# Kernel tuning notes

Measured on AMD Instinct MI355X. Metric: run time of the kernel, lower is better.

Reference implementation:

```python
import jax, jax.numpy as jnp
import numpy as np

N, LT, LV, D, H = 4, 1024, 1024, 1024, 16
HD = D // H
EPS = 1e-12


def layernorm(x, w, b):
    u = x.mean(-1, keepdims=True)
    s = ((x - u) ** 2).mean(-1, keepdims=True)
    return w * (x - u) / jnp.sqrt(s + EPS) + b


def attention(q_in, k_in, v_in, mask, qw, qb, kw, kb, vw, vb):
    # mask: (N, Lq_or_1, Lk) float in {0,1}; torch Linear is x @ W.T + b
    def heads(x, w, b):
        y = x @ w.T + b
        return y.reshape(y.shape[0], y.shape[1], H, HD).transpose(0, 2, 1, 3)  # (N,H,L,hd)
    q, k, v = heads(q_in, qw, qb), heads(k_in, kw, kb), heads(v_in, vw, vb)
    scores = jnp.einsum('bhqd,bhkd->bhqk', q, k) / np.sqrt(HD).astype(np.float32)
    scores = scores + (1.0 - mask[:, None]) * (-10000.0)
    probs = jax.nn.softmax(scores, axis=-1)  # dropout is identity in eval
    ctx = jnp.einsum('bhqk,bhkd->bhqd', probs, v)
    return ctx.transpose(0, 2, 1, 3).reshape(q_in.shape[0], q_in.shape[1], D)


def setup_inputs() -> dict:
    key = jax.random.key(0)
    ks = jax.random.split(key, 16)
    inp = {
        'dec_hidden_states': jax.random.normal(ks[0], (N, LT, D), jnp.float32),
        'enc_outputs': jax.random.normal(ks[1], (N, LV, D), jnp.float32),
        'dec_mask': jnp.ones((N, LT), jnp.float32),
        'enc_mask': jnp.ones((N, LV), jnp.float32),
    }
    wnames = ['sa_qw', 'sa_kw', 'sa_vw', 'ca_qw', 'ca_kw', 'ca_vw', 'out_w']
    for i, n in enumerate(wnames):
        inp[n] = jax.random.normal(ks[2 + i], (D, D), jnp.float32) * 0.02
    for n in ['sa_qb', 'sa_kb', 'sa_vb', 'ca_qb', 'ca_kb', 'ca_vb', 'out_b', 'n1_b', 'n2_b', 'out_ln_b']:
        inp[n] = jnp.zeros((D,), jnp.float32)
    for n in ['n1_w', 'n2_w', 'out_ln_w']:
        inp[n] = jnp.ones((D,), jnp.float32)
    return inp


def reference(dec_hidden_states, enc_outputs, dec_mask, enc_mask,
              sa_qw, sa_qb, sa_kw, sa_kb, sa_vw, sa_vb, n1_w, n1_b,
              ca_qw, ca_qb, ca_kw, ca_kb, ca_vw, ca_vb, n2_w, n2_b,
              out_w, out_b, out_ln_w, out_ln_b):
    Lt = dec_mask.shape[1]
    # diagonal_mask=True: causal tril combined with padding mask
    self_mask = dec_mask[:, None, :] * jnp.tril(jnp.ones((Lt, Lt), dec_mask.dtype))  # (N,Lt,Lt)
    a = attention(dec_hidden_states, dec_hidden_states, dec_hidden_states, self_mask,
                  sa_qw, sa_qb, sa_kw, sa_kb, sa_vw, sa_vb)
    a = layernorm(a + dec_hidden_states, n1_w, n1_b)
    c = attention(a, enc_outputs, enc_outputs, enc_mask[:, None, :],
                  ca_qw, ca_qb, ca_kw, ca_kb, ca_vw, ca_vb)
    c = layernorm(a + c, n2_w, n2_b)
    # BertOutput called as output(x, x): dense, residual, LN (dropout = identity)
    h = c @ out_w.T + out_b
    return layernorm(h + c, out_ln_w, out_ln_b)
```

## Files before the change

### kernel.cpp

```cpp
#include <hip/hip_runtime.h>
#include <cstdint>
#include <cstddef>

typedef __bf16 bf16x8 __attribute__((ext_vector_type(8)));
typedef float  floatx4 __attribute__((ext_vector_type(4)));
typedef unsigned short ushortx8 __attribute__((ext_vector_type(8)));
typedef unsigned short ushortx4 __attribute__((ext_vector_type(4)));

#define MFMA16(a, b, c) __builtin_amdgcn_mfma_f32_16x16x32_bf16((a), (b), (c), 0, 0, 0)

__device__ inline unsigned short f2bf(float f) {
    unsigned int u = __float_as_uint(f);
    unsigned int r = (u + 0x7fffu + ((u >> 16) & 1u)) >> 16;
    return (unsigned short)r;
}
__device__ inline float bf2f(unsigned short u) {
    return __uint_as_float(((unsigned int)u) << 16);
}

struct Src2 { const float* p[2]; };
__global__ __launch_bounds__(256) void k_x2_to_bf16(Src2 s2, unsigned short* __restrict__ dst) {
    int i = blockIdx.x * 256 + threadIdx.x;
    const float* src = s2.p[i >> 19];
    int off = i & 524287;
    const float4* s = (const float4*)src + (size_t)off * 2;
    float4 x0 = s[0], x1 = s[1];
    ushortx8 o;
    o[0] = f2bf(x0.x); o[1] = f2bf(x0.y); o[2] = f2bf(x0.z); o[3] = f2bf(x0.w);
    o[4] = f2bf(x1.x); o[5] = f2bf(x1.y); o[6] = f2bf(x1.z); o[7] = f2bf(x1.w);
    *((ushortx8*)dst + i) = o;
}
struct Src7 { const float* p[7]; };
__global__ __launch_bounds__(256) void k_w7_to_bf16(Src7 s7, unsigned short* __restrict__ dst) {
    int i = blockIdx.x * 256 + threadIdx.x;
    const float* src = s7.p[i >> 17];
    int off = i & 131071;
    const float4* s = (const float4*)src + (size_t)off * 2;
    float4 x0 = s[0], x1 = s[1];
    ushortx8 o;
    o[0] = f2bf(x0.x); o[1] = f2bf(x0.y); o[2] = f2bf(x0.z); o[3] = f2bf(x0.w);
    o[4] = f2bf(x1.x); o[5] = f2bf(x1.y); o[6] = f2bf(x1.z); o[7] = f2bf(x1.w);
    *((ushortx8*)dst + i) = o;
}

template <int MODE>
__global__ __launch_bounds__(256) void k_gemm_bias(const unsigned short* __restrict__ A,
                                                   const unsigned short* __restrict__ A2,
                                                   const unsigned short* __restrict__ W,
                                                   const float* __restrict__ bias0,
                                                   const float* __restrict__ bias1,
                                                   const float* __restrict__ bias2,
                                                   void* __restrict__ d0,
                                                   void* __restrict__ d1,
                                                   void* __restrict__ d2,
                                                   int K) {
    __shared__ __align__(16) unsigned short As[128 * 32];
    __shared__ __align__(16) unsigned short Bs[128 * 32];
    const int tid = threadIdx.x;
    const int wave = tid >> 6, lane = tid & 63;
    const int quad = lane >> 4, l15 = lane & 15;
    const int wm = wave >> 1, wn = wave & 1;
    const int m0 = blockIdx.x * 128, n0 = blockIdx.y * 128;
    const int sect_blk = n0 >> 10;

    const unsigned short* Ause = (MODE == 4 && sect_blk != 0) ? A2 : A;

    const size_t rowbytes = (size_t)K * 2;
    const int idx0 = tid, idx1 = 256 + tid;
    const int rA0 = idx0 >> 2, cb0 = (idx0 & 3) << 4;
    const int rA1 = idx1 >> 2, cb1 = (idx1 & 3) << 4;
    const char* gA0 = (const char*)Ause + (size_t)(m0 + rA0) * rowbytes + cb0;
    const char* gA1 = (const char*)Ause + (size_t)(m0 + rA1) * rowbytes + cb1;
    const char* gB0 = (const char*)W + (size_t)(n0 + rA0) * rowbytes + cb0;
    const char* gB1 = (const char*)W + (size_t)(n0 + rA1) * rowbytes + cb1;

    int4 pa0 = *(const int4*)gA0, pa1 = *(const int4*)gA1;
    int4 pb0 = *(const int4*)gB0, pb1 = *(const int4*)gB1;

    floatx4 acc[4][4] = {};

    const int KT = K >> 5;
    for (int kt = 0; kt < KT; ++kt) {
        __syncthreads();
        ((int4*)As)[idx0] = pa0; ((int4*)As)[idx1] = pa1;
        ((int4*)Bs)[idx0] = pb0; ((int4*)Bs)[idx1] = pb1;
        __syncthreads();
        if (kt + 1 < KT) {
            gA0 += 64; gA1 += 64; gB0 += 64; gB1 += 64;
            pa0 = *(const int4*)gA0; pa1 = *(const int4*)gA1;
            pb0 = *(const int4*)gB0; pb1 = *(const int4*)gB1;
        }
        bf16x8 af[4], bfr[4];
        const char* Asb = (const char*)As;
        const char* Bsb = (const char*)Bs;
#pragma unroll
        for (int r = 0; r < 4; ++r)
            af[r] = *(const bf16x8*)(Asb + ((wm * 64 + r * 16 + l15) * 64 + quad * 16));
#pragma unroll
        for (int c = 0; c < 4; ++c)
            bfr[c] = *(const bf16x8*)(Bsb + ((wn * 64 + c * 16 + l15) * 64 + quad * 16));
#pragma unroll
        for (int r = 0; r < 4; ++r)
#pragma unroll
            for (int c = 0; c < 4; ++c)
                acc[r][c] = MFMA16(af[r], bfr[c], acc[r][c]);
    }

#pragma unroll
    for (int c = 0; c < 4; ++c) {
        int col = n0 + wn * 64 + c * 16 + l15;
        int sect = col >> 10, cc = col & 1023;
        float bv;
        if (MODE == 3) bv = bias0[col];
        else bv = (sect == 0 ? bias0 : (sect == 1 ? bias1 : bias2))[cc];
        int h = cc >> 6, d = cc & 63;
#pragma unroll
        for (int r = 0; r < 4; ++r) {
            int mrow = m0 + wm * 64 + r * 16 + quad * 4;
#pragma unroll
            for (int i = 0; i < 4; ++i) {
                float v = acc[r][c][i] + bv;
                int row = mrow + i;
                if (MODE == 3) {
                    ((float*)d0)[(size_t)row * 1024 + col] = v;
                } else {
                    int b = row >> 10, l = row & 1023;
                    unsigned short* base = (unsigned short*)(sect == 0 ? d0 : (sect == 1 ? d1 : d2));
                    bool isV = (sect == 2);
                    size_t off;
                    if (isV) off = (size_t)(b * 16 + h) * 65536 + (size_t)(l >> 5) * 2048 + d * 32 + (l & 31);
                    else off = ((size_t)(b * 16 + h) * 1024 + l) * 64 + d;
                    base[off] = f2bf(v);
                }
            }
        }
    }
}

__global__ __launch_bounds__(256) void k_flash_attn(const unsigned short* __restrict__ Qp,
                                                    const unsigned short* __restrict__ Kp,
                                                    const unsigned short* __restrict__ Vp,
                                                    const float* __restrict__ mask,
                                                    float* __restrict__ ctx,
                                                    int causal) {
    const int L = 1024, D = 1024;
    int f = blockIdx.x;
    int qi = ((f >> 3) + (f >> 7)) & 15;
    int bh = (f & 7) + ((f >> 7) << 3);
    int h = bh & 15, b = bh >> 4;
    int tid = threadIdx.x;
    int wave = tid >> 6, lane = tid & 63, quad = lane >> 4, l15 = lane & 15;
    int qbase = qi * 64 + wave * 16;

    __shared__ __align__(16) unsigned short Ks[4096];
    __shared__ __align__(16) unsigned short Vs[5120];
    __shared__ unsigned short penb[1024];
    __shared__ __align__(16) unsigned short Plds[4][1280];

    {
        float4 mv = ((const float4*)(mask + b * L))[tid];
        ushortx4 pv;
        pv[0] = f2bf((1.0f - mv.x) * -10000.0f);
        pv[1] = f2bf((1.0f - mv.y) * -10000.0f);
        pv[2] = f2bf((1.0f - mv.z) * -10000.0f);
        pv[3] = f2bf((1.0f - mv.w) * -10000.0f);
        *((ushortx4*)penb + tid) = pv;
    }

    const unsigned short* Qh = Qp + ((size_t)(b * 16 + h) * 1024 + qbase) * 64;
    bf16x8 qf0 = *(const bf16x8*)(Qh + l15 * 64 + quad * 8);
    bf16x8 qf1 = *(const bf16x8*)(Qh + l15 * 64 + 32 + quad * 8);

    const char* Kh = (const char*)(Kp + (size_t)(b * 16 + h) * 65536);
    const char* Vh = (const char*)(Vp + (size_t)(b * 16 + h) * 65536);

    int ktiles = causal ? (qi + 1) : 16;

    char* Ksb = (char*)Ks;
    char* Vsb = (char*)Vs;
    int krow = tid >> 3, kblk = tid & 7;
    int kd0 = krow * 128 + ((kblk ^ (krow & 7)) << 4);
    int kd1 = kd0 + 32 * 128;
    int vd0 = (tid >> 2) * 80 + ((tid & 3) << 4);
    int vd1 = vd0 + 5120;

    int karA[4], karB[4];
#pragma unroll
    for (int r = 0; r < 4; ++r) {
        int row = r * 16 + l15;
        karA[r] = row * 128 + ((quad ^ (l15 & 7)) << 4);
        karB[r] = row * 128 + (((quad | 4) ^ (l15 & 7)) << 4);
    }
    int var_[8];
#pragma unroll
    for (int s = 0; s < 2; ++s)
#pragma unroll
        for (int fi = 0; fi < 4; ++fi)
            var_[s * 4 + fi] = s * 5120 + (fi * 16 + l15) * 80 + (quad << 4);

    floatx4 O[4] = {};
    float lsum[4] = {0.f, 0.f, 0.f, 0.f};
    unsigned short* pw_lo = &Plds[wave][0];
    unsigned short* pw_hi = &Plds[wave][640];

    int4 ka0 = *(const int4*)(Kh + tid * 16);
    int4 ka1 = *(const int4*)(Kh + 4096 + tid * 16);
    int4 va0 = *(const int4*)(Vh + tid * 16);
    int4 va1 = *(const int4*)(Vh + 4096 + tid * 16);

    for (int kt = 0; kt < ktiles; ++kt) {
        *(int4*)(Ksb + kd0) = ka0;
        *(int4*)(Ksb + kd1) = ka1;
        *(int4*)(Vsb + vd0) = va0;
        *(int4*)(Vsb + vd1) = va1;
        __syncthreads();
        if (kt + 1 < ktiles) {
            const char* Kg = Kh + (size_t)(kt + 1) * 8192;
            const char* Vg = Vh + (size_t)(kt + 1) * 8192;
            ka0 = *(const int4*)(Kg + tid * 16);
            ka1 = *(const int4*)(Kg + 4096 + tid * 16);
            va0 = *(const int4*)(Vg + tid * 16);
            va1 = *(const int4*)(Vg + 4096 + tid * 16);
        }
        int k0 = kt * 64;

        floatx4 S0 = {}, S1 = {}, S2 = {}, S3 = {};
        {
            bf16x8 kA0 = *(const bf16x8*)(Ksb + karA[0]);
            bf16x8 kB0 = *(const bf16x8*)(Ksb + karB[0]);
            bf16x8 kA1 = *(const bf16x8*)(Ksb + karA[1]);
            bf16x8 kB1 = *(const bf16x8*)(Ksb + karB[1]);
            S0 = MFMA16(qf0, kA0, S0); S0 = MFMA16(qf1, kB0, S0);
            S1 = MFMA16(qf0, kA1, S1); S1 = MFMA16(qf1, kB1, S1);
            bf16x8 kA2 = *(const bf16x8*)(Ksb + karA[2]);
            bf16x8 kB2 = *(const bf16x8*)(Ksb + karB[2]);
            bf16x8 kA3 = *(const bf16x8*)(Ksb + karA[3]);
            bf16x8 kB3 = *(const bf16x8*)(Ksb + karB[3]);
            S2 = MFMA16(qf0, kA2, S2); S2 = MFMA16(qf1, kB2, S2);
            S3 = MFMA16(qf0, kA3, S3); S3 = MFMA16(qf1, kB3, S3);
        }

        float pen0 = bf2f(penb[k0 + l15]);
        float pen1 = bf2f(penb[k0 + 16 + l15]);
        float pen2 = bf2f(penb[k0 + 32 + l15]);
        float pen3 = bf2f(penb[k0 + 48 + l15]);

#pragma unroll
        for (int i = 0; i < 4; ++i) {
            float e0, e1, e2, e3;
            if (causal) {
                int q = qbase + quad * 4 + i;
                e0 = ((k0 + l15) <= q) ? pen0 : -10000.0f;
                e1 = ((k0 + 16 + l15) <= q) ? pen1 : -10000.0f;
                e2 = ((k0 + 32 + l15) <= q) ? pen2 : -10000.0f;
                e3 = ((k0 + 48 + l15) <= q) ? pen3 : -10000.0f;
            } else {
                e0 = pen0; e1 = pen1; e2 = pen2; e3 = pen3;
            }
            float p0 = __expf(fmaf(S0[i], 0.125f, e0));
            float p1 = __expf(fmaf(S1[i], 0.125f, e1));
            float p2 = __expf(fmaf(S2[i], 0.125f, e2));
            float p3 = __expf(fmaf(S3[i], 0.125f, e3));
            lsum[i] += (p0 + p1) + (p2 + p3);
            int ro = (quad * 4 + i) * 40;
            pw_lo[ro + l15] = f2bf(p0);
            pw_lo[ro + 16 + l15] = f2bf(p1);
            pw_hi[ro + l15] = f2bf(p2);
            pw_hi[ro + 16 + l15] = f2bf(p3);
        }

        bf16x8 pa_lo = *(const bf16x8*)(pw_lo + l15 * 40 + quad * 8);
        bf16x8 pa_hi = *(const bf16x8*)(pw_hi + l15 * 40 + quad * 8);
        bf16x8 v0 = *(const bf16x8*)(Vsb + var_[0]);
        bf16x8 v1 = *(const bf16x8*)(Vsb + var_[1]);
        bf16x8 v2 = *(const bf16x8*)(Vsb + var_[2]);
        bf16x8 v3 = *(const bf16x8*)(Vsb + var_[3]);
        O[0] = MFMA16(pa_lo, v0, O[0]);
        O[1] = MFMA16(pa_lo, v1, O[1]);
        O[2] = MFMA16(pa_lo, v2, O[2]);
        O[3] = MFMA16(pa_lo, v3, O[3]);
        bf16x8 v4 = *(const bf16x8*)(Vsb + var_[4]);
        bf16x8 v5 = *(const bf16x8*)(Vsb + var_[5]);
        bf16x8 v6 = *(const bf16x8*)(Vsb + var_[6]);
        bf16x8 v7 = *(const bf16x8*)(Vsb + var_[7]);
        O[0] = MFMA16(pa_hi, v4, O[0]);
        O[1] = MFMA16(pa_hi, v5, O[1]);
        O[2] = MFMA16(pa_hi, v6, O[2]);
        O[3] = MFMA16(pa_hi, v7, O[3]);
        __syncthreads();
    }

#pragma unroll
    for (int i = 0; i < 4; ++i) {
        float l = lsum[i];
        l += __shfl_xor(l, 1);
        l += __shfl_xor(l, 2);
        l += __shfl_xor(l, 4);
        l += __shfl_xor(l, 8);
        float inv = 1.0f / l;
        int q = qbase + quad * 4 + i;
        float* op = ctx + ((size_t)(b * L + q)) * D + h * 64;
#pragma unroll
        for (int fi = 0; fi < 4; ++fi) op[fi * 16 + l15] = O[fi][i] * inv;
    }
}

__global__ __launch_bounds__(256) void k_add_ln(const float* __restrict__ X,
                                                const float* __restrict__ Y,
                                                const float* __restrict__ w,
                                                const float* __restrict__ bvec,
                                                float* __restrict__ outf,
                                                unsigned short* __restrict__ outbf) {
    int row = blockIdx.x;
    int tid = threadIdx.x;
    float4 x = *((const float4*)(X + (size_t)row * 1024) + tid);
    float4 y = *((const float4*)(Y + (size_t)row * 1024) + tid);
    float v0 = x.x + y.x, v1 = x.y + y.y, v2 = x.z + y.z, v3 = x.w + y.w;
    float s = v0 + v1 + v2 + v3;
    float s2 = v0 * v0 + v1 * v1 + v2 * v2 + v3 * v3;
#pragma unroll
    for (int off = 32; off > 0; off >>= 1) {
        s += __shfl_xor(s, off);
        s2 += __shfl_xor(s2, off);
    }
    __shared__ float red[8];
    int wave = tid >> 6, lane = tid & 63;
    if (lane == 0) { red[wave] = s; red[4 + wave] = s2; }
    __syncthreads();
    s = red[0] + red[1] + red[2] + red[3];
    s2 = red[4] + red[5] + red[6] + red[7];
    float u = s * (1.0f / 1024.0f);
    float var = s2 * (1.0f / 1024.0f) - u * u;
    float r = 1.0f / sqrtf(fmaxf(var, 0.0f) + 1e-12f);
    float4 wv = *((const float4*)w + tid);
    float4 bv = *((const float4*)bvec + tid);
    float o0 = wv.x * (v0 - u) * r + bv.x;
    float o1 = wv.y * (v1 - u) * r + bv.y;
    float o2 = wv.z * (v2 - u) * r + bv.z;
    float o3 = wv.w * (v3 - u) * r + bv.w;
    float4 o = {o0, o1, o2, o3};
    *((float4*)(outf + (size_t)row * 1024) + tid) = o;
    if (outbf) {
        ushortx4 ob;
        ob[0] = f2bf(o0); ob[1] = f2bf(o1); ob[2] = f2bf(o2); ob[3] = f2bf(o3);
        *((ushortx4*)outbf + (size_t)row * 256 + tid) = ob;
    }
}

extern "C" void kernel_launch(void* const* d_in, const int* in_sizes, int n_in,
                              void* d_out, int out_size, void* d_ws, size_t ws_size,
                              hipStream_t stream) {
    (void)in_sizes; (void)n_in; (void)out_size; (void)ws_size;
    const float* dec = (const float*)d_in[0];
    const float* enc = (const float*)d_in[1];
    const float* dec_mask = (const float*)d_in[2];
    const float* enc_mask = (const float*)d_in[3];
    const float* b_saq = (const float*)d_in[11];
    const float* b_sak = (const float*)d_in[12];
    const float* b_sav = (const float*)d_in[13];
    const float* b_caq = (const float*)d_in[14];
    const float* b_cak = (const float*)d_in[15];
    const float* b_cav = (const float*)d_in[16];
    const float* b_out = (const float*)d_in[17];
    const float* n1_b = (const float*)d_in[18];
    const float* n2_b = (const float*)d_in[19];
    const float* oln_b = (const float*)d_in[20];
    const float* n1_w = (const float*)d_in[21];
    const float* n2_w = (const float*)d_in[22];
    const float* oln_w = (const float*)d_in[23];

    char* ws = (char*)d_ws;
    const size_t MB2 = 2097152;
    const size_t ACT_BF = 8388608;
    const size_t ACT_F32 = 16777216;
    unsigned short* Wbf[7];
    for (int i = 0; i < 7; ++i) Wbf[i] = (unsigned short*)(ws + i * MB2);
    size_t off = 7 * MB2;
    unsigned short* Xbf = (unsigned short*)(ws + off); off += ACT_BF;
    unsigned short* Ebf = (unsigned short*)(ws + off); off += ACT_BF;
    unsigned short* Abf = (unsigned short*)(ws + off); off += ACT_BF;
    unsigned short* Cbf = (unsigned short*)(ws + off); off += ACT_BF;
    unsigned short* Qp = (unsigned short*)(ws + off); off += ACT_BF;
    unsigned short* Kp = (unsigned short*)(ws + off); off += ACT_BF;
    unsigned short* Vp = (unsigned short*)(ws + off); off += ACT_BF;
    float* ctx = (float*)(ws + off); off += ACT_F32;
    float* a_f32 = (float*)(ws + off); off += ACT_F32;
    float* c_f32 = (float*)(ws + off); off += ACT_F32;
    float* h_f32 = ctx;
    float* outp = (float*)d_out;

    dim3 blk(256);
    dim3 attn_grid(1024);

    Src2 s2; s2.p[0] = dec; s2.p[1] = enc;
    k_x2_to_bf16<<<dim3(4096), blk, 0, stream>>>(s2, Xbf);
    Src7 s7;
    for (int i = 0; i < 7; ++i) s7.p[i] = (const float*)d_in[4 + i];
    k_w7_to_bf16<<<dim3(3584), blk, 0, stream>>>(s7, Wbf[0]);

    k_gemm_bias<0><<<dim3(32, 24), blk, 0, stream>>>(Xbf, Xbf, Wbf[0], b_saq, b_sak, b_sav,
                                                     Qp, Kp, Vp, 1024);
    k_flash_attn<<<attn_grid, blk, 0, stream>>>(Qp, Kp, Vp, dec_mask, ctx, 1);
    k_add_ln<<<dim3(4096), blk, 0, stream>>>(ctx, dec, n1_w, n1_b, a_f32, Abf);

    k_gemm_bias<4><<<dim3(32, 24), blk, 0, stream>>>(Abf, Ebf, Wbf[3], b_caq, b_cak, b_cav,
                                                     Qp, Kp, Vp, 1024);
    k_flash_attn<<<attn_grid, blk, 0, stream>>>(Qp, Kp, Vp, enc_mask, ctx, 0);
    k_add_ln<<<dim3(4096), blk, 0, stream>>>(a_f32, ctx, n2_w, n2_b, c_f32, Cbf);

    k_gemm_bias<3><<<dim3(32, 8), blk, 0, stream>>>(Cbf, Cbf, Wbf[6], b_out, b_out, b_out,
                                                    h_f32, nullptr, nullptr, 1024);
    k_add_ln<<<dim3(4096), blk, 0, stream>>>(h_f32, c_f32, oln_w, oln_b, outp, (unsigned short*)nullptr);
}
```

Baseline: 351.0 us.

## Double query rows per attention wave, reuse K/V fragments, use exp2 softmax

The flash-attention kernel now handles 128 query rows per block (32 per wave, split into two 16-row halves). Each K/V fragment loaded from LDS is reused for both halves, and the grid is halved. Softmax switches to exp2 with a log2e-prescaled score and float mask penalty. P is packed into bf16 pairs with a perm instruction, and V is stored with a permuted key order to match. Causal tiles and halves that are fully masked are skipped. The risk is higher register pressure, hence launch_bounds(256,2), and fewer blocks for the GPU to schedule.

```diff
diff --git a/kernel.cpp b/kernel.cpp
--- a/kernel.cpp
+++ b/kernel.cpp
@@ -13,9 +13,6 @@
     unsigned int u = __float_as_uint(f);
     unsigned int r = (u + 0x7fffu + ((u >> 16) & 1u)) >> 16;
     return (unsigned short)r;
-}
-__device__ inline float bf2f(unsigned short u) {
-    return __uint_as_float(((unsigned int)u) << 16);
 }
 
 struct Src2 { const float* p[2]; };
@@ -128,8 +125,13 @@
                     unsigned short* base = (unsigned short*)(sect == 0 ? d0 : (sect == 1 ? d1 : d2));
                     bool isV = (sect == 2);
                     size_t off;
-                    if (isV) off = (size_t)(b * 16 + h) * 65536 + (size_t)(l >> 5) * 2048 + d * 32 + (l & 31);
-                    else off = ((size_t)(b * 16 + h) * 1024 + l) * 64 + d;
+                    if (isV) {
+                        int kk = l & 31;
+                        int kperm = ((kk & 15) << 1) | (kk >> 4);
+                        off = (size_t)(b * 16 + h) * 65536 + (size_t)(l >> 5) * 2048 + d * 32 + kperm;
+                    } else {
+                        off = ((size_t)(b * 16 + h) * 1024 + l) * 64 + d;
+                    }
                     base[off] = f2bf(v);
                 }
             }
@@ -137,44 +139,50 @@
     }
 }
 
-__global__ __launch_bounds__(256) void k_flash_attn(const unsigned short* __restrict__ Qp,
-                                                    const unsigned short* __restrict__ Kp,
-                                                    const unsigned short* __restrict__ Vp,
-                                                    const float* __restrict__ mask,
-                                                    float* __restrict__ ctx,
-                                                    int causal) {
+__global__ __launch_bounds__(256, 2) void k_flash_attn(const unsigned short* __restrict__ Qp,
+                                                       const unsigned short* __restrict__ Kp,
+                                                       const unsigned short* __restrict__ Vp,
+                                                       const float* __restrict__ mask,
+                                                       float* __restrict__ ctx,
+                                                       int causal) {
     const int L = 1024, D = 1024;
+    const float SC = 0.18033688011112042f;
     int f = blockIdx.x;
-    int qi = ((f >> 3) + (f >> 7)) & 15;
-    int bh = (f & 7) + ((f >> 7) << 3);
+    int g = f >> 6;
+    int bh = (f & 7) + (g << 3);
+    int qt = ((f >> 3) + g) & 7;
     int h = bh & 15, b = bh >> 4;
     int tid = threadIdx.x;
     int wave = tid >> 6, lane = tid & 63, quad = lane >> 4, l15 = lane & 15;
-    int qbase = qi * 64 + wave * 16;
+    int qbase = qt * 128 + wave * 32;
 
     __shared__ __align__(16) unsigned short Ks[4096];
     __shared__ __align__(16) unsigned short Vs[5120];
-    __shared__ unsigned short penb[1024];
-    __shared__ __align__(16) unsigned short Plds[4][1280];
+    __shared__ float penf[1024];
+    __shared__ __align__(16) unsigned short Plds[4 * 1280];
 
     {
         float4 mv = ((const float4*)(mask + b * L))[tid];
-        ushortx4 pv;
-        pv[0] = f2bf((1.0f - mv.x) * -10000.0f);
-        pv[1] = f2bf((1.0f - mv.y) * -10000.0f);
-        pv[2] = f2bf((1.0f - mv.z) * -10000.0f);
-        pv[3] = f2bf((1.0f - mv.w) * -10000.0f);
-        *((ushortx4*)penb + tid) = pv;
+        float4 pv;
+        pv.x = (1.0f - mv.x) * -14426.950408889634f;
+        pv.y = (1.0f - mv.y) * -14426.950408889634f;
+        pv.z = (1.0f - mv.z) * -14426.950408889634f;
+        pv.w = (1.0f - mv.w) * -14426.950408889634f;
+        ((float4*)penf)[tid] = pv;
     }
 
     const unsigned short* Qh = Qp + ((size_t)(b * 16 + h) * 1024 + qbase) * 64;
-    bf16x8 qf0 = *(const bf16x8*)(Qh + l15 * 64 + quad * 8);
-    bf16x8 qf1 = *(const bf16x8*)(Qh + l15 * 64 + 32 + quad * 8);
+    bf16x8 qf[2][2];
+#pragma unroll
+    for (int qh = 0; qh < 2; ++qh) {
+        qf[qh][0] = *(const bf16x8*)(Qh + (qh * 16 + l15) * 64 + quad * 8);
+        qf[qh][1] = *(const bf16x8*)(Qh + (qh * 16 + l15) * 64 + 32 + quad * 8);
+    }
 
     const char* Kh = (const char*)(Kp + (size_t)(b * 16 + h) * 65536);
     const char* Vh = (const char*)(Vp + (size_t)(b * 16 + h) * 65536);
 
-    int ktiles = causal ? (qi + 1) : 16;
+    int ktiles = causal ? (2 * qt + 2) : 16;
 
     char* Ksb = (char*)Ks;
     char* Vsb = (char*)Vs;
@@ -198,10 +206,10 @@
         for (int fi = 0; fi < 4; ++fi)
             var_[s * 4 + fi] = s * 5120 + (fi * 16 + l15) * 80 + (quad << 4);
 
-    floatx4 O[4] = {};
-    float lsum[4] = {0.f, 0.f, 0.f, 0.f};
-    unsigned short* pw_lo = &Plds[wave][0];
-    unsigned short* pw_hi = &Plds[wave][640];
+    floatx4 O[2][4] = {};
+    float lsum[2][4] = {};
+    unsigned short* pw = &Plds[wave * 1280];
+    unsigned int* pw32 = (unsigned int*)pw;
 
     int4 ka0 = *(const int4*)(Kh + tid * 16);
     int4 ka1 = *(const int4*)(Kh + 4096 + tid * 16);
@@ -224,85 +232,92 @@
         }
         int k0 = kt * 64;
 
-        floatx4 S0 = {}, S1 = {}, S2 = {}, S3 = {};
-        {
-            bf16x8 kA0 = *(const bf16x8*)(Ksb + karA[0]);
-            bf16x8 kB0 = *(const bf16x8*)(Ksb + karB[0]);
-            bf16x8 kA1 = *(const bf16x8*)(Ksb + karA[1]);
-            bf16x8 kB1 = *(const bf16x8*)(Ksb + karB[1]);
-            S0 = MFMA16(qf0, kA0, S0); S0 = MFMA16(qf1, kB0, S0);
-            S1 = MFMA16(qf0, kA1, S1); S1 = MFMA16(qf1, kB1, S1);
-            bf16x8 kA2 = *(const bf16x8*)(Ksb + karA[2]);
-            bf16x8 kB2 = *(const bf16x8*)(Ksb + karB[2]);
-            bf16x8 kA3 = *(const bf16x8*)(Ksb + karA[3]);
-            bf16x8 kB3 = *(const bf16x8*)(Ksb + karB[3]);
-            S2 = MFMA16(qf0, kA2, S2); S2 = MFMA16(qf1, kB2, S2);
-            S3 = MFMA16(qf0, kA3, S3); S3 = MFMA16(qf1, kB3, S3);
+        if (!(causal && k0 > qbase + 31)) {
+            bf16x8 kA[4], kB[4];
+#pragma unroll
+            for (int r = 0; r < 4; ++r) {
+                kA[r] = *(const bf16x8*)(Ksb + karA[r]);
+                kB[r] = *(const bf16x8*)(Ksb + karB[r]);
+            }
+            bf16x8 vv[8];
+#pragma unroll
+            for (int s = 0; s < 8; ++s) vv[s] = *(const bf16x8*)(Vsb + var_[s]);
+            float pr0 = penf[k0 + l15];
+            float pr1 = penf[k0 + 16 + l15];
+            float pr2 = penf[k0 + 32 + l15];
+            float pr3 = penf[k0 + 48 + l15];
+
+#pragma unroll
+            for (int qh = 0; qh < 2; ++qh) {
+                int qlo = qbase + qh * 16;
+                if (causal && k0 > qlo + 15) continue;
+                bool boundary = causal && (k0 + 63 > qlo);
+
+                floatx4 S0 = {}, S1 = {}, S2 = {}, S3 = {};
+                S0 = MFMA16(qf[qh][0], kA[0], S0); S0 = MFMA16(qf[qh][1], kB[0], S0);
+                S1 = MFMA16(qf[qh][0], kA[1], S1); S1 = MFMA16(qf[qh][1], kB[1], S1);
+                S2 = MFMA16(qf[qh][0], kA[2], S2); S2 = MFMA16(qf[qh][1], kB[2], S2);
+                S3 = MFMA16(qf[qh][0], kA[3], S3); S3 = MFMA16(qf[qh][1], kB[3], S3);
+
+                int qrow = qlo + quad * 4;
+#pragma unroll
+                for (int i = 0; i < 4; ++i) {
+                    float x0 = fmaf(S0[i], SC, pr0);
+                    float x1 = fmaf(S1[i], SC, pr1);
+                    float x2 = fmaf(S2[i], SC, pr2);
+                    float x3 = fmaf(S3[i], SC, pr3);
+                    if (boundary) {
+                        int q = qrow + i;
+                        x0 = ((k0 + l15) <= q) ? x0 : -50000.0f;
+                        x1 = ((k0 + 16 + l15) <= q) ? x1 : -50000.0f;
+                        x2 = ((k0 + 32 + l15) <= q) ? x2 : -50000.0f;
+                        x3 = ((k0 + 48 + l15) <= q) ? x3 : -50000.0f;
+                    }
+                    float p0 = __builtin_amdgcn_exp2f(x0);
+                    float p1 = __builtin_amdgcn_exp2f(x1);
+                    float p2 = __builtin_amdgcn_exp2f(x2);
+                    float p3 = __builtin_amdgcn_exp2f(x3);
+                    lsum[qh][i] += (p0 + p1) + (p2 + p3);
+                    unsigned r0 = __float_as_uint(p0) + 0x8000u;
+                    unsigned r1 = __float_as_uint(p1) + 0x8000u;
+                    unsigned r2 = __float_as_uint(p2) + 0x8000u;
+                    unsigned r3 = __float_as_uint(p3) + 0x8000u;
+                    unsigned plo = __builtin_amdgcn_perm(r1, r0, 0x07060302u);
+                    unsigned phi = __builtin_amdgcn_perm(r3, r2, 0x07060302u);
+                    int ro = (quad * 4 + i) * 20;
+                    pw32[ro + l15] = plo;
+                    pw32[320 + ro + l15] = phi;
+                }
+                bf16x8 pa_lo = *(const bf16x8*)(pw + l15 * 40 + quad * 8);
+                bf16x8 pa_hi = *(const bf16x8*)(pw + 640 + l15 * 40 + quad * 8);
+                O[qh][0] = MFMA16(pa_lo, vv[0], O[qh][0]);
+                O[qh][1] = MFMA16(pa_lo, vv[1], O[qh][1]);
+                O[qh][2] = MFMA16(pa_lo, vv[2], O[qh][2]);
+                O[qh][3] = MFMA16(pa_lo, vv[3], O[qh][3]);
+                O[qh][0] = MFMA16(pa_hi, vv[4], O[qh][0]);
+                O[qh][1] = MFMA16(pa_hi, vv[5], O[qh][1]);
+                O[qh][2] = MFMA16(pa_hi, vv[6], O[qh][2]);
+                O[qh][3] = MFMA16(pa_hi, vv[7], O[qh][3]);
+            }
         }
-
-        float pen0 = bf2f(penb[k0 + l15]);
-        float pen1 = bf2f(penb[k0 + 16 + l15]);
-        float pen2 = bf2f(penb[k0 + 32 + l15]);
-        float pen3 = bf2f(penb[k0 + 48 + l15]);
-
+        __syncthreads();
+    }
+
+#pragma unroll
+    for (int qh = 0; qh < 2; ++qh)
 #pragma unroll
         for (int i = 0; i < 4; ++i) {
-            float e0, e1, e2, e3;
-            if (causal) {
-                int q = qbase + quad * 4 + i;
-                e0 = ((k0 + l15) <= q) ? pen0 : -10000.0f;
-                e1 = ((k0 + 16 + l15) <= q) ? pen1 : -10000.0f;
-                e2 = ((k0 + 32 + l15) <= q) ? pen2 : -10000.0f;
-                e3 = ((k0 + 48 + l15) <= q) ? pen3 : -10000.0f;
-            } else {
-                e0 = pen0; e1 = pen1; e2 = pen2; e3 = pen3;
-            }
-            float p0 = __expf(fmaf(S0[i], 0.125f, e0));
-            float p1 = __expf(fmaf(S1[i], 0.125f, e1));
-            float p2 = __expf(fmaf(S2[i], 0.125f, e2));
-            float p3 = __expf(fmaf(S3[i], 0.125f, e3));
-            lsum[i] += (p0 + p1) + (p2 + p3);
-            int ro = (quad * 4 + i) * 40;
-            pw_lo[ro + l15] = f2bf(p0);
-            pw_lo[ro + 16 + l15] = f2bf(p1);
-            pw_hi[ro + l15] = f2bf(p2);
-            pw_hi[ro + 16 + l15] = f2bf(p3);
+            float l = lsum[qh][i];
+            l += __shfl_xor(l, 1);
+            l += __shfl_xor(l, 2);
+            l += __shfl_xor(l, 4);
+            l += __shfl_xor(l, 8);
+            float inv = 1.0f / l;
+            int q = qbase + qh * 16 + quad * 4 + i;
+            float* op = ctx + ((size_t)(b * L + q)) * D + h * 64;
+#pragma unroll
+            for (int fi = 0; fi < 4; ++fi) op[fi * 16 + l15] = O[qh][fi][i] * inv;
         }
-
-        bf16x8 pa_lo = *(const bf16x8*)(pw_lo + l15 * 40 + quad * 8);
-        bf16x8 pa_hi = *(const bf16x8*)(pw_hi + l15 * 40 + quad * 8);
-        bf16x8 v0 = *(const bf16x8*)(Vsb + var_[0]);
-        bf16x8 v1 = *(const bf16x8*)(Vsb + var_[1]);
-        bf16x8 v2 = *(const bf16x8*)(Vsb + var_[2]);
-        bf16x8 v3 = *(const bf16x8*)(Vsb + var_[3]);
-        O[0] = MFMA16(pa_lo, v0, O[0]);
-        O[1] = MFMA16(pa_lo, v1, O[1]);
-        O[2] = MFMA16(pa_lo, v2, O[2]);
-        O[3] = MFMA16(pa_lo, v3, O[3]);
-        bf16x8 v4 = *(const bf16x8*)(Vsb + var_[4]);
-        bf16x8 v5 = *(const bf16x8*)(Vsb + var_[5]);
-        bf16x8 v6 = *(const bf16x8*)(Vsb + var_[6]);
-        bf16x8 v7 = *(const bf16x8*)(Vsb + var_[7]);
-        O[0] = MFMA16(pa_hi, v4, O[0]);
-        O[1] = MFMA16(pa_hi, v5, O[1]);
-        O[2] = MFMA16(pa_hi, v6, O[2]);
-        O[3] = MFMA16(pa_hi, v7, O[3]);
-        __syncthreads();
-    }
-
-#pragma unroll
-    for (int i = 0; i < 4; ++i) {
-        float l = lsum[i];
-        l += __shfl_xor(l, 1);
-        l += __shfl_xor(l, 2);
-        l += __shfl_xor(l, 4);
-        l += __shfl_xor(l, 8);
-        float inv = 1.0f / l;
-        int q = qbase + quad * 4 + i;
-        float* op = ctx + ((size_t)(b * L + q)) * D + h * 64;
-#pragma unroll
-        for (int fi = 0; fi < 4; ++fi) op[fi * 16 + l15] = O[fi][i] * inv;
-    }
 }
 
 __global__ __launch_bounds__(256) void k_add_ln(const float* __restrict__ X,
@@ -390,7 +405,7 @@
     float* outp = (float*)d_out;
 
     dim3 blk(256);
-    dim3 attn_grid(1024);
+    dim3 attn_grid(512);
 
     Src2 s2; s2.p[0] = dec; s2.p[1] = enc;
     k_x2_to_bf16<<<dim3(4096), blk, 0, stream>>>(s2, Xbf);
```

New measurement: 337.6 us. -3.8%, faster.
